# Performance work log

Hardware: AMD Instinct MI355X
Metric: run time of the kernel (lower is better)

## Reference

```python
import jax, jax.numpy as jnp
import numpy as np

N_STARS = 4096
N_DIC = 4096
N_FEAT = 16  # (d_max+1)(d_max+2)/2 + graph_features = 10 + 6
OPD_DIM = 256
BATCH = 2048


def setup_inputs() -> dict:
    key = jax.random.key(0)
    k1, k2, k3, k4, k5 = jax.random.split(key, 5)
    # Observed star positions in the FoV (x_lims/y_lims = [0, 4096]).
    obs_pos = jax.random.uniform(k1, (N_STARS, 2), dtype=jnp.float32) * 4096.0
    # Query positions MUST be exact rows of obs_pos (the layer does an
    # exact-equality search); take a random subset of stars.
    perm = jax.random.permutation(k2, N_STARS)[:BATCH]
    positions = obs_pos[perm]
    spatial_dic = jax.random.normal(k3, (N_STARS, N_DIC), dtype=jnp.float32)
    alpha_mat = jax.random.normal(k4, (N_DIC, N_FEAT), dtype=jnp.float32)
    # S initialized uniform in [-1e-3, 1e-3] in the original layer.
    S_mat = (jax.random.uniform(k5, (N_FEAT, OPD_DIM, OPD_DIM), dtype=jnp.float32) * 2.0 - 1.0) * 1e-3
    return {
        "positions": positions,
        "obs_pos": obs_pos,
        "spatial_dic": spatial_dic,
        "alpha_mat": alpha_mat,
        "S_mat": S_mat,
    }


def _lookup_indices(positions, obs_pos):
    # Faithful to tf.where(tf.equal(obs_pos, pos))[0, 0]: elementwise equality
    # against the full (n_stars, 2) table, take the row of the FIRST matching
    # element in row-major order.
    eq = positions[:, None, :] == obs_pos[None, :, :]          # [batch, n_stars, 2]
    flat = eq.reshape(eq.shape[0], -1)                          # [batch, n_stars*2]
    first = jnp.argmax(flat, axis=1)                            # first True, row-major
    return first // 2                                           # row index -> int


def reference(positions, obs_pos, spatial_dic, alpha_mat, S_mat):
    indices = _lookup_indices(positions, obs_pos)               # [batch]
    batch_dict = jnp.take(spatial_dic, indices, axis=0)         # [batch, n_dic]
    inter = batch_dict @ alpha_mat                              # [batch, n_feat]
    # tensordot over the feature axis -> [batch, opd_dim, opd_dim]
    return jnp.einsum("bf,fij->bij", inter, S_mat)
```

## Files before the change

kernel.cpp:

```cpp
#include <hip/hip_runtime.h>
#include <cstdint>

#define NSTARS 4096
#define NDIC   4096
#define NFEAT  16
#define NPIX   65536
#define BATCH  2048
#define RPB    8
#define BPB    256

using f32x4 = __attribute__((ext_vector_type(4))) float;

__global__ __launch_bounds__(256) void k_inter(
    const float*  __restrict__ positions,
    const float2* __restrict__ obs,
    const float*  __restrict__ spatial,
    const float*  __restrict__ alpha,
    float*        __restrict__ inter)
{
    __shared__ int   s_idx[RPB];
    __shared__ float s_red[4 * RPB * NFEAT];

    const int tid  = threadIdx.x;
    const int lane = tid & 63;
    const int wave = tid >> 6;
    const int b0   = blockIdx.x * RPB;

    if (tid < RPB) s_idx[tid] = 0x7FFFFFFF;
    __syncthreads();

    float px[RPB], py[RPB];
    #pragma unroll
    for (int b = 0; b < RPB; ++b) {
        px[b] = positions[(b0 + b) * 2 + 0];
        py[b] = positions[(b0 + b) * 2 + 1];
    }
    for (int s = tid; s < NSTARS; s += 256) {
        float2 o = obs[s];
        #pragma unroll
        for (int b = 0; b < RPB; ++b) {
            if (px[b] == o.x || py[b] == o.y) atomicMin(&s_idx[b], s);
        }
    }
    __syncthreads();

    int idx[RPB];
    #pragma unroll
    for (int b = 0; b < RPB; ++b) {
        int v = s_idx[b];
        idx[b] = (v == 0x7FFFFFFF) ? 0 : v;
    }

    float acc[RPB][NFEAT];
    #pragma unroll
    for (int b = 0; b < RPB; ++b)
        #pragma unroll
        for (int f = 0; f < NFEAT; ++f) acc[b][f] = 0.0f;

    const float4* alpha4 = (const float4*)alpha;

    #pragma unroll
    for (int step = 0; step < 4; ++step) {
        const int d0 = tid * 4 + step * 1024;
        float4 v[RPB];
        #pragma unroll
        for (int b = 0; b < RPB; ++b)
            v[b] = *(const float4*)(spatial + (size_t)idx[b] * NDIC + d0);

        #pragma unroll
        for (int k = 0; k < 4; ++k) {
            const float4 a0 = alpha4[(size_t)(d0 + k) * 4 + 0];
            const float4 a1 = alpha4[(size_t)(d0 + k) * 4 + 1];
            const float4 a2 = alpha4[(size_t)(d0 + k) * 4 + 2];
            const float4 a3 = alpha4[(size_t)(d0 + k) * 4 + 3];
            #pragma unroll
            for (int b = 0; b < RPB; ++b) {
                const float vb = (&v[b].x)[k];
                acc[b][0]  += vb * a0.x;  acc[b][1]  += vb * a0.y;
                acc[b][2]  += vb * a0.z;  acc[b][3]  += vb * a0.w;
                acc[b][4]  += vb * a1.x;  acc[b][5]  += vb * a1.y;
                acc[b][6]  += vb * a1.z;  acc[b][7]  += vb * a1.w;
                acc[b][8]  += vb * a2.x;  acc[b][9]  += vb * a2.y;
                acc[b][10] += vb * a2.z;  acc[b][11] += vb * a2.w;
                acc[b][12] += vb * a3.x;  acc[b][13] += vb * a3.y;
                acc[b][14] += vb * a3.z;  acc[b][15] += vb * a3.w;
            }
        }
    }

    #pragma unroll
    for (int off = 1; off < 64; off <<= 1)
        #pragma unroll
        for (int b = 0; b < RPB; ++b)
            #pragma unroll
            for (int f = 0; f < NFEAT; ++f)
                acc[b][f] += __shfl_xor(acc[b][f], off);

    if (lane == 0) {
        #pragma unroll
        for (int b = 0; b < RPB; ++b)
            #pragma unroll
            for (int f = 0; f < NFEAT; f += 4)
                *(float4*)&s_red[(wave * RPB + b) * NFEAT + f] =
                    make_float4(acc[b][f], acc[b][f+1], acc[b][f+2], acc[b][f+3]);
    }
    __syncthreads();

    if (tid < RPB * NFEAT) {
        const int r = tid >> 4, f = tid & 15;
        float x = s_red[(0 * RPB + r) * NFEAT + f]
                + s_red[(1 * RPB + r) * NFEAT + f]
                + s_red[(2 * RPB + r) * NFEAT + f]
                + s_red[(3 * RPB + r) * NFEAT + f];
        inter[(size_t)(b0 + r) * NFEAT + f] = x;
    }
}

__global__ __launch_bounds__(256) void k_opd(
    const float* __restrict__ interw,
    const f32x4* __restrict__ S4,
    f32x4*       __restrict__ out4)
{
    const int tid   = threadIdx.x;
    const int chunk = blockIdx.x & 63;
    const int bg    = blockIdx.x >> 6;
    const int p4    = chunk * 256 + tid;

    f32x4 s[NFEAT];
    #pragma unroll
    for (int f = 0; f < NFEAT; ++f)
        s[f] = S4[(size_t)f * (NPIX / 4) + p4];

    const float* w = interw + (size_t)bg * BPB * NFEAT;
    f32x4* o = out4 + (size_t)bg * BPB * (NPIX / 4) + p4;

    for (int g = 0; g < BPB / 4; ++g) {
        f32x4 acc[4];
        #pragma unroll
        for (int b = 0; b < 4; ++b) {
            const float* wr = w + (size_t)(g * 4 + b) * NFEAT;
            f32x4 a = s[0] * wr[0];
            a += s[1]  * wr[1];   a += s[2]  * wr[2];   a += s[3]  * wr[3];
            a += s[4]  * wr[4];   a += s[5]  * wr[5];   a += s[6]  * wr[6];
            a += s[7]  * wr[7];   a += s[8]  * wr[8];   a += s[9]  * wr[9];
            a += s[10] * wr[10];  a += s[11] * wr[11];  a += s[12] * wr[12];
            a += s[13] * wr[13];  a += s[14] * wr[14];  a += s[15] * wr[15];
            acc[b] = a;
        }
        #pragma unroll
        for (int b = 0; b < 4; ++b)
            __builtin_nontemporal_store(acc[b],
                o + (size_t)(g * 4 + b) * (NPIX / 4));
    }
}

extern "C" void kernel_launch(void* const* d_in, const int* in_sizes, int n_in,
                              void* d_out, int out_size, void* d_ws, size_t ws_size,
                              hipStream_t stream) {
    const float*  positions = (const float*)d_in[0];
    const float2* obs       = (const float2*)d_in[1];
    const float*  spatial   = (const float*)d_in[2];
    const float*  alpha     = (const float*)d_in[3];
    const f32x4*  S4        = (const f32x4*)d_in[4];
    f32x4*        out       = (f32x4*)d_out;
    float*        inter     = (float*)d_ws;

    k_inter<<<BATCH / RPB, 256, 0, stream>>>(positions, obs, spatial, alpha, inter);
    k_opd<<<(NPIX / 1024) * (BATCH / BPB), 256, 0, stream>>>(
        inter, S4, out);
}
```

Baseline: 131.8 us.

## Split k_inter dictionary reduction across two blocks, sum partials in k_opd

The dictionary dimension of the gather-matmul is split into two halves, and each half is handled by a separate block, so k_inter launches twice as many blocks and each does half the loads. The two partial inter vectors go to workspace, and k_opd adds them before the feature contraction. This raises parallelism in the first kernel, which ran only 256 blocks on a device with many CUs. The cost is that the position lookup runs twice and k_opd does extra scalar loads.

```diff
diff --git a/kernel.cpp b/kernel.cpp
--- a/kernel.cpp
+++ b/kernel.cpp
@@ -16,7 +16,7 @@
     const float2* __restrict__ obs,
     const float*  __restrict__ spatial,
     const float*  __restrict__ alpha,
-    float*        __restrict__ inter)
+    float*        __restrict__ partial)
 {
     __shared__ int   s_idx[RPB];
     __shared__ float s_red[4 * RPB * NFEAT];
@@ -24,7 +24,8 @@
     const int tid  = threadIdx.x;
     const int lane = tid & 63;
     const int wave = tid >> 6;
-    const int b0   = blockIdx.x * RPB;
+    const int seg  = blockIdx.x & 1;
+    const int b0   = (blockIdx.x >> 1) * RPB;
 
     if (tid < RPB) s_idx[tid] = 0x7FFFFFFF;
     __syncthreads();
@@ -60,8 +61,8 @@
     const float4* alpha4 = (const float4*)alpha;
 
     #pragma unroll
-    for (int step = 0; step < 4; ++step) {
-        const int d0 = tid * 4 + step * 1024;
+    for (int step = 0; step < 2; ++step) {
+        const int d0 = seg * 2048 + step * 1024 + tid * 4;
         float4 v[RPB];
         #pragma unroll
         for (int b = 0; b < RPB; ++b)
@@ -112,12 +113,12 @@
                 + s_red[(1 * RPB + r) * NFEAT + f]
                 + s_red[(2 * RPB + r) * NFEAT + f]
                 + s_red[(3 * RPB + r) * NFEAT + f];
-        inter[(size_t)(b0 + r) * NFEAT + f] = x;
+        partial[((size_t)seg * BATCH + (b0 + r)) * NFEAT + f] = x;
     }
 }
 
 __global__ __launch_bounds__(256) void k_opd(
-    const float* __restrict__ interw,
+    const float* __restrict__ part,
     const f32x4* __restrict__ S4,
     f32x4*       __restrict__ out4)
 {
@@ -131,20 +132,26 @@
     for (int f = 0; f < NFEAT; ++f)
         s[f] = S4[(size_t)f * (NPIX / 4) + p4];
 
-    const float* w = interw + (size_t)bg * BPB * NFEAT;
+    const float* w0 = part + (size_t)bg * BPB * NFEAT;
+    const float* w1 = w0 + (size_t)BATCH * NFEAT;
     f32x4* o = out4 + (size_t)bg * BPB * (NPIX / 4) + p4;
 
     for (int g = 0; g < BPB / 4; ++g) {
         f32x4 acc[4];
         #pragma unroll
         for (int b = 0; b < 4; ++b) {
-            const float* wr = w + (size_t)(g * 4 + b) * NFEAT;
-            f32x4 a = s[0] * wr[0];
-            a += s[1]  * wr[1];   a += s[2]  * wr[2];   a += s[3]  * wr[3];
-            a += s[4]  * wr[4];   a += s[5]  * wr[5];   a += s[6]  * wr[6];
-            a += s[7]  * wr[7];   a += s[8]  * wr[8];   a += s[9]  * wr[9];
-            a += s[10] * wr[10];  a += s[11] * wr[11];  a += s[12] * wr[12];
-            a += s[13] * wr[13];  a += s[14] * wr[14];  a += s[15] * wr[15];
+            const size_t ro = (size_t)(g * 4 + b) * NFEAT;
+            const float* wa = w0 + ro;
+            const float* wb = w1 + ro;
+            float wf[NFEAT];
+            #pragma unroll
+            for (int f = 0; f < NFEAT; ++f) wf[f] = wa[f] + wb[f];
+            f32x4 a = s[0] * wf[0];
+            a += s[1]  * wf[1];   a += s[2]  * wf[2];   a += s[3]  * wf[3];
+            a += s[4]  * wf[4];   a += s[5]  * wf[5];   a += s[6]  * wf[6];
+            a += s[7]  * wf[7];   a += s[8]  * wf[8];   a += s[9]  * wf[9];
+            a += s[10] * wf[10];  a += s[11] * wf[11];  a += s[12] * wf[12];
+            a += s[13] * wf[13];  a += s[14] * wf[14];  a += s[15] * wf[15];
             acc[b] = a;
         }
         #pragma unroll
@@ -163,9 +170,9 @@
     const float*  alpha     = (const float*)d_in[3];
     const f32x4*  S4        = (const f32x4*)d_in[4];
     f32x4*        out       = (f32x4*)d_out;
-    float*        inter     = (float*)d_ws;
+    float*        partial   = (float*)d_ws;
 
-    k_inter<<<BATCH / RPB, 256, 0, stream>>>(positions, obs, spatial, alpha, inter);
+    k_inter<<<(BATCH / RPB) * 2, 256, 0, stream>>>(positions, obs, spatial, alpha, partial);
     k_opd<<<(NPIX / 1024) * (BATCH / BPB), 256, 0, stream>>>(
-        inter, S4, out);
+        partial, S4, out);
 }
```

After: 145.3 us. 10.3% more time.
